# Optimization experiments

Measured on AMD Instinct MI355X. Metric: run time of the kernel, lower is better.

Reference implementation:

```python
import jax, jax.numpy as jnp
import numpy as np

N = 50000      # nodes
E = 800000     # edges (avg degree 16)
H = 4          # heads
C = 64         # per-head dim (= hidden_dim, TransformerConv out_channels)
D = H * C      # 256, concat output dim
VOCAB = 100


def setup_inputs() -> dict:
    key = jax.random.key(0)
    ks = jax.random.split(key, 16)
    f = lambda k, shape: (jax.random.normal(k, shape, jnp.float32) * 0.05)
    return {
        "x": jax.random.randint(ks[0], (N,), 0, VOCAB),
        "edge_index": jax.random.randint(ks[1], (2, E), 0, N),
        "embed": f(ks[2], (VOCAB, C)),        # node_embed table (hidden_dim=64)
        "Wq": f(ks[3], (C, D)), "bq": f(ks[4], (D,)),
        "Wk": f(ks[5], (C, D)), "bk": f(ks[6], (D,)),
        "Wv": f(ks[7], (C, D)), "bv": f(ks[8], (D,)),
        "Wskip": f(ks[9], (C, D)), "bskip": f(ks[10], (D,)),
        "Wbeta": f(ks[11], (3 * D, 1)),       # lin_beta has no bias in PyG
        "Wcoop": f(ks[12], (D, 1)), "bcoop": f(ks[13], (1,)),
        "Wanom": f(ks[14], (D, 1)), "banom": f(ks[15], (1,)),
    }


def _segment_softmax(logits, seg, num_segments):
    # logits: [E, H], seg: [E] destination-node ids
    m = jax.ops.segment_max(logits, seg, num_segments=num_segments)   # [N, H]
    ex = jnp.exp(logits - m[seg])
    s = jax.ops.segment_sum(ex, seg, num_segments=num_segments)       # [N, H]
    return ex / (s[seg] + 1e-16)


def _transformer_conv(h, src, dst, Wq, bq, Wk, bk, Wv, bv, Wskip, bskip, Wbeta):
    # h: [N, C] node features; src->dst edges; PyG TransformerConv(beta=True)
    q = (h @ Wq + bq).reshape(N, H, C)
    k = (h @ Wk + bk).reshape(N, H, C)
    v = (h @ Wv + bv).reshape(N, H, C)
    # per-edge attention logits: query of dst, key of src
    logits = (q[dst] * k[src]).sum(-1) / np.sqrt(C)    # [E, H]
    alpha = _segment_softmax(logits, dst, N)           # softmax over in-edges of dst
    msg = v[src] * alpha[..., None]                    # [E, H, C]
    out = jax.ops.segment_sum(msg, dst, num_segments=N).reshape(N, D)
    # beta-gated skip connection
    x_r = h @ Wskip + bskip                            # [N, D]
    beta = jax.nn.sigmoid(jnp.concatenate([out, x_r, out - x_r], axis=-1) @ Wbeta)
    return beta * x_r + (1.0 - beta) * out             # [N, D]


def reference(x, edge_index, embed, Wq, bq, Wk, bk, Wv, bv,
              Wskip, bskip, Wbeta, Wcoop, bcoop, Wanom, banom):
    h = embed[x]                                       # long input -> embedding
    src, dst = edge_index[0], edge_index[1]
    h = _transformer_conv(h, src, dst, Wq, bq, Wk, bk, Wv, bv, Wskip, bskip, Wbeta)
    h = jax.nn.relu(h)                                 # dropout is identity (eval)
    cooperation = jax.nn.sigmoid(h @ Wcoop + bcoop)    # [N, 1]
    anomaly = jax.nn.sigmoid(h @ Wanom + banom)        # [N, 1]
    return cooperation, anomaly, h
```

## Files before the change

### kernel.cpp

```cpp
#include <hip/hip_runtime.h>
#include <hip/hip_bf16.h>

typedef __hip_bfloat16 bf16;

#define NN 50000
#define EE 800000
#define VOCABSZ 100
#define DD 256
#define NW 25
#define MAXD 64
#define NBUCK 500
#define BNODES 100
#define AWG 512
#define PCAP 24

static __device__ __forceinline__ float b2f(bf16 v) { return __bfloat162float(v); }

static __device__ __forceinline__ float ldf(const void* p, int i, int isf32) {
  if (isf32) return ((const float*)p)[i];
  return b2f(((const bf16*)p)[i]);
}

static __device__ __forceinline__ int block_detect(const unsigned short* e16) {
  __shared__ int f;
  if (threadIdx.x == 0) f = 0;
  __syncthreads();
  unsigned int ex = (e16[threadIdx.x] >> 7) & 0xFF;
  unsigned long long any = __ballot(ex >= 128);
  if ((threadIdx.x & 63) == 0 && any) atomicOr(&f, 1);
  __syncthreads();
  return f;
}

__global__ void k_build_tables(const void* __restrict__ embed,
    const void* __restrict__ Wq, const void* __restrict__ bq,
    const void* __restrict__ Wk, const void* __restrict__ bk,
    const void* __restrict__ Wv, const void* __restrict__ bv,
    const void* __restrict__ Ws, const void* __restrict__ bs,
    const void* __restrict__ Wbeta,
    const void* __restrict__ Wcoop, const void* __restrict__ bcoop,
    const void* __restrict__ Wanom, const void* __restrict__ banom,
    float* __restrict__ Qt, float* __restrict__ Kt,
    bf16* __restrict__ VtH, bf16* __restrict__ StH,
    float* __restrict__ Wf, int* __restrict__ flag)
{
  __shared__ float e[64];
  int isf32 = block_detect((const unsigned short*)embed);
  int t = threadIdx.x;

  if (blockIdx.y == 4) {
    if (blockIdx.x != 0) return;
    Wf[t]       = ldf(Wbeta, t, isf32)       + ldf(Wbeta, 512 + t, isf32);
    Wf[256 + t] = ldf(Wbeta, 256 + t, isf32) - ldf(Wbeta, 512 + t, isf32);
    Wf[512 + t] = ldf(Wcoop, t, isf32);
    Wf[768 + t] = ldf(Wanom, t, isf32);
    if (t == 0) {
      Wf[1024] = ldf(bcoop, 0, isf32);
      Wf[1025] = ldf(banom, 0, isf32);
      flag[0] = isf32;
    }
    return;
  }

  int row = blockIdx.x;
  if (t < 64) e[t] = ldf(embed, row * 64 + t, isf32);
  __syncthreads();
  const void* W; const void* b;
  switch (blockIdx.y) {
    case 0:  W = Wq; b = bq; break;
    case 1:  W = Wk; b = bk; break;
    case 2:  W = Wv; b = bv; break;
    default: W = Ws; b = bs; break;
  }
  float acc;
  if (isf32) {
    const float* w32 = (const float*)W;
    acc = ((const float*)b)[t];
    #pragma unroll 8
    for (int c = 0; c < 64; ++c) acc = fmaf(e[c], w32[c * DD + t], acc);
  } else {
    const bf16* w16 = (const bf16*)W;
    acc = b2f(((const bf16*)b)[t]);
    #pragma unroll 8
    for (int c = 0; c < 64; ++c) acc = fmaf(e[c], b2f(w16[c * DD + t]), acc);
  }
  switch (blockIdx.y) {
    case 0:  Qt[row * DD + t] = acc; break;
    case 1:  Kt[row * DD + t] = acc; break;
    case 2:  VtH[row * DD + t] = __float2bfloat16(acc); break;
    default: StH[row * DD + t] = __float2bfloat16(acc); break;
  }
}

__global__ void k_build_logits(const float* __restrict__ Qt, const float* __restrict__ Kt,
                               float* __restrict__ Et)
{
  __shared__ float q[DD];
  int a = blockIdx.x;
  q[threadIdx.x] = Qt[a * DD + threadIdx.x];
  __syncthreads();
  for (int idx = threadIdx.x; idx < VOCABSZ * 4; idx += 256) {
    int b = idx >> 2, h = idx & 3;
    const float* kk = Kt + b * DD + h * 64;
    const float* qq = q + h * 64;
    float acc = 0.f;
    #pragma unroll 8
    for (int c = 0; c < 64; ++c) acc += qq[c] * kk[c];
    Et[(a * VOCABSZ + b) * 4 + h] = __expf(acc * 0.125f);
  }
}

__global__ __launch_bounds__(256) void k_scatter2(
    const int* __restrict__ src, const int* __restrict__ dst,
    const int* __restrict__ x,
    unsigned char* __restrict__ cnt, unsigned short* __restrict__ seg)
{
  __shared__ unsigned int cur[NBUCK];
  const int t = threadIdx.x;
  for (int i = t; i < NBUCK; i += 256) cur[i] = 0;
  __syncthreads();
  const int per = (EE + AWG - 1) / AWG;
  const int e0 = blockIdx.x * per;
  int e1 = e0 + per; if (e1 > EE) e1 = EE;
  const size_t wbase = (size_t)blockIdx.x * NBUCK;
  for (int i = e0 + t; i < e1; i += 256) {
    unsigned d = (unsigned)dst[i];
    unsigned b = d / (unsigned)BNODES;
    unsigned dl = d - b * BNODES;
    unsigned xv = (unsigned)x[src[i]];
    unsigned pos = atomicAdd(&cur[b], 1u);
    if (pos < PCAP)
      seg[(wbase + b) * PCAP + pos] = (unsigned short)(dl | (xv << 7));
  }
  __syncthreads();
  for (int i = t; i < NBUCK; i += 256) {
    unsigned c = cur[i]; if (c > PCAP) c = PCAP;
    cnt[wbase + i] = (unsigned char)c;
  }
}

__global__ __launch_bounds__(256) void k_lists(
    const unsigned char* __restrict__ cnt, const unsigned short* __restrict__ seg,
    int* __restrict__ deg, unsigned short* __restrict__ ell16)
{
  __shared__ unsigned int hist[BNODES * NW];
  const int b = blockIdx.x;
  const int t = threadIdx.x;
  for (int i = t; i < BNODES * NW; i += 256) hist[i] = 0;
  __syncthreads();
  for (int w = t; w < AWG; w += 256) {
    const size_t sbase = ((size_t)w * NBUCK + b);
    unsigned c = cnt[sbase];
    const unsigned short* sp = seg + sbase * PCAP;
    for (unsigned i = 0; i < c; ++i) {
      unsigned r = sp[i];
      unsigned dl = r & 127u, xv = r >> 7;
      atomicAdd(&hist[dl * NW + (xv >> 2)], 1u << ((xv & 3) * 8));
    }
  }
  __syncthreads();
  if (t < BNODES) {
    int n = b * BNODES + t;
    const unsigned int* cw = hist + t * NW;
    unsigned short* dp = ell16 + (size_t)n * MAXD;
    int k = 0;
    #pragma unroll
    for (int w = 0; w < NW; ++w) {
      unsigned word = cw[w];
      if (!word) continue;
      #pragma unroll
      for (int bb = 0; bb < 4; ++bb) {
        unsigned c = (word >> (8 * bb)) & 255u;
        if (c) { if (k < MAXD) dp[k] = (unsigned short)((unsigned)(w * 4 + bb) | (c << 8)); k++; }
      }
    }
    deg[n] = (k < MAXD) ? k : MAXD;
  }
}

__global__ __launch_bounds__(256) void k_node(
    const int* __restrict__ x, const int* __restrict__ deg,
    const unsigned short* __restrict__ ell16,
    const bf16* __restrict__ VtH, const bf16* __restrict__ StH,
    const float* __restrict__ Et, const float* __restrict__ Wf,
    void* __restrict__ out, const int* __restrict__ flag)
{
  const int t = threadIdx.x;
  const int lane = t & 63;
  const int wv = t >> 6;
  const int l31 = lane & 31;
  const int hbase = lane & 32;
  const int n = blockIdx.x * 8 + wv * 2 + (lane >> 5);
  const int cb = l31 << 3;
  const int head = l31 >> 3;

  const int xd = x[n];
  const int dgn = deg[n];
  const int dgA = __shfl(dgn, 0, 64);
  const int dgB = __shfl(dgn, 32, 64);
  const int dmax = max(dgA, dgB);

  unsigned int mye = (l31 < dgn) ? (unsigned int)ell16[(size_t)n * MAXD + l31] : 0u;

  union BF8U { uint4 u; bf16 h[8]; };
  BF8U xru; xru.u = *reinterpret_cast<const uint4*>(StH + xd * DD + cb);
  const float4 wo0 = *reinterpret_cast<const float4*>(Wf + cb);
  const float4 wo1 = *reinterpret_cast<const float4*>(Wf + cb + 4);
  const float4 wx0 = *reinterpret_cast<const float4*>(Wf + 256 + cb);
  const float4 wx1 = *reinterpret_cast<const float4*>(Wf + 256 + cb + 4);

  const float* __restrict__ Erow = Et + xd * (VOCABSZ * 4) + head;

  float s = 0.f;
  float o0 = 0.f, o1 = 0.f, o2 = 0.f, o3 = 0.f;
  float o4 = 0.f, o5 = 0.f, o6 = 0.f, o7 = 0.f;

  const int j1 = (dmax < 32) ? dmax : 32;
  #pragma unroll 4
  for (int j = 0; j < j1; ++j) {
    unsigned int en = (unsigned int)__shfl((int)mye, hbase + j, 64);
    int xs = (int)(en & 255u);
    float e = (float)(en >> 8) * Erow[xs << 2];
    s += e;
    BF8U vv; vv.u = *reinterpret_cast<const uint4*>(VtH + xs * DD + cb);
    o0 = fmaf(e, b2f(vv.h[0]), o0); o1 = fmaf(e, b2f(vv.h[1]), o1);
    o2 = fmaf(e, b2f(vv.h[2]), o2); o3 = fmaf(e, b2f(vv.h[3]), o3);
    o4 = fmaf(e, b2f(vv.h[4]), o4); o5 = fmaf(e, b2f(vv.h[5]), o5);
    o6 = fmaf(e, b2f(vv.h[6]), o6); o7 = fmaf(e, b2f(vv.h[7]), o7);
  }
  if (dmax > 32) {
    unsigned int mye2 = (l31 + 32 < dgn) ? (unsigned int)ell16[(size_t)n * MAXD + 32 + l31] : 0u;
    for (int j = 32; j < dmax; ++j) {
      unsigned int en = (unsigned int)__shfl((int)mye2, hbase + (j - 32), 64);
      int xs = (int)(en & 255u);
      float e = (float)(en >> 8) * Erow[xs << 2];
      s += e;
      BF8U vv; vv.u = *reinterpret_cast<const uint4*>(VtH + xs * DD + cb);
      o0 = fmaf(e, b2f(vv.h[0]), o0); o1 = fmaf(e, b2f(vv.h[1]), o1);
      o2 = fmaf(e, b2f(vv.h[2]), o2); o3 = fmaf(e, b2f(vv.h[3]), o3);
      o4 = fmaf(e, b2f(vv.h[4]), o4); o5 = fmaf(e, b2f(vv.h[5]), o5);
      o6 = fmaf(e, b2f(vv.h[6]), o6); o7 = fmaf(e, b2f(vv.h[7]), o7);
    }
  }

  const float inv = 1.f / (s + 1e-16f);
  float o[8] = { o0*inv, o1*inv, o2*inv, o3*inv, o4*inv, o5*inv, o6*inv, o7*inv };
  float xr[8];
  #pragma unroll
  for (int j = 0; j < 8; ++j) xr[j] = b2f(xru.h[j]);

  float bp = o[0]*wo0.x + o[1]*wo0.y + o[2]*wo0.z + o[3]*wo0.w
           + o[4]*wo1.x + o[5]*wo1.y + o[6]*wo1.z + o[7]*wo1.w
           + xr[0]*wx0.x + xr[1]*wx0.y + xr[2]*wx0.z + xr[3]*wx0.w
           + xr[4]*wx1.x + xr[5]*wx1.y + xr[6]*wx1.z + xr[7]*wx1.w;
  #pragma unroll
  for (int m = 16; m >= 1; m >>= 1) bp += __shfl_xor(bp, m, 64);
  const float beta = 1.f / (1.f + __expf(-bp));

  const float4 wc0 = *reinterpret_cast<const float4*>(Wf + 512 + cb);
  const float4 wc1 = *reinterpret_cast<const float4*>(Wf + 512 + cb + 4);
  const float4 wa0 = *reinterpret_cast<const float4*>(Wf + 768 + cb);
  const float4 wa1 = *reinterpret_cast<const float4*>(Wf + 768 + cb + 4);
  const float wcv[8] = { wc0.x, wc0.y, wc0.z, wc0.w, wc1.x, wc1.y, wc1.z, wc1.w };
  const float wav[8] = { wa0.x, wa0.y, wa0.z, wa0.w, wa1.x, wa1.y, wa1.z, wa1.w };

  float h[8];
  float pc = 0.f, pa = 0.f;
  #pragma unroll
  for (int j = 0; j < 8; ++j) {
    float hv = beta * xr[j] + (1.f - beta) * o[j];
    hv = fmaxf(hv, 0.f);
    h[j] = hv;
    pc = fmaf(hv, wcv[j], pc);
    pa = fmaf(hv, wav[j], pa);
  }
  #pragma unroll
  for (int m = 16; m >= 1; m >>= 1) {
    pc += __shfl_xor(pc, m, 64);
    pa += __shfl_xor(pa, m, 64);
  }
  const float coop = 1.f / (1.f + __expf(-(pc + Wf[1024])));
  const float anom = 1.f / (1.f + __expf(-(pa + Wf[1025])));

  if (flag[0]) {
    float* fo = (float*)out;
    if (l31 == 0) { fo[n] = coop; fo[NN + n] = anom; }
    float4* hp = reinterpret_cast<float4*>(fo + 2 * NN + (size_t)n * DD + cb);
    hp[0] = make_float4(h[0], h[1], h[2], h[3]);
    hp[1] = make_float4(h[4], h[5], h[6], h[7]);
  } else {
    bf16* bo = (bf16*)out;
    if (l31 == 0) { bo[n] = __float2bfloat16(coop); bo[NN + n] = __float2bfloat16(anom); }
    struct alignas(16) BF8S { bf16 v[8]; } hb;
    #pragma unroll
    for (int j = 0; j < 8; ++j) hb.v[j] = __float2bfloat16(h[j]);
    *reinterpret_cast<BF8S*>(bo + 2 * NN + (size_t)n * DD + cb) = hb;
  }
}

extern "C" void kernel_launch(void* const* d_in, const int* in_sizes, int n_in,
                              void* d_out, int out_size, void* d_ws, size_t ws_size,
                              hipStream_t stream) {
  (void)in_sizes; (void)n_in; (void)out_size; (void)ws_size;
  const int*  x     = (const int*)d_in[0];
  const int*  ei    = (const int*)d_in[1];
  const void* embed = d_in[2];
  const void* Wq = d_in[3];  const void* bq = d_in[4];
  const void* Wk = d_in[5];  const void* bk = d_in[6];
  const void* Wv = d_in[7];  const void* bv = d_in[8];
  const void* Ws = d_in[9];  const void* bs = d_in[10];
  const void* Wbeta = d_in[11];
  const void* Wcoop = d_in[12]; const void* bcoop = d_in[13];
  const void* Wanom = d_in[14]; const void* banom = d_in[15];
  const int* src = ei;
  const int* dst = ei + EE;

  char* base = (char*)d_ws;
  size_t pos = 0;
  auto take = [&](size_t bytes) -> char* {
    char* p = base + pos;
    pos = (pos + bytes + 255) & ~(size_t)255;
    return p;
  };
  float* Qt  = (float*)take(VOCABSZ * DD * sizeof(float));
  float* Kt  = (float*)take(VOCABSZ * DD * sizeof(float));
  bf16*  VtH = (bf16*)take(VOCABSZ * DD * sizeof(bf16));
  bf16*  StH = (bf16*)take(VOCABSZ * DD * sizeof(bf16));
  float* Et  = (float*)take(VOCABSZ * VOCABSZ * 4 * sizeof(float));
  float* Wf  = (float*)take(1026 * sizeof(float));
  int*   deg = (int*)take(NN * sizeof(int));
  int*   flag= (int*)take(256 * sizeof(int));
  unsigned char*  cnt   = (unsigned char*)take((size_t)AWG * NBUCK);
  unsigned short* seg   = (unsigned short*)take((size_t)AWG * NBUCK * PCAP * sizeof(unsigned short));
  unsigned short* ell16 = (unsigned short*)take((size_t)NN * MAXD * sizeof(unsigned short));

  k_build_tables<<<dim3(VOCABSZ, 5), 256, 0, stream>>>(
      embed, Wq, bq, Wk, bk, Wv, bv, Ws, bs,
      Wbeta, Wcoop, bcoop, Wanom, banom,
      Qt, Kt, VtH, StH, Wf, flag);
  k_build_logits<<<VOCABSZ, 256, 0, stream>>>(Qt, Kt, Et);

  k_scatter2<<<AWG, 256, 0, stream>>>(src, dst, x, cnt, seg);
  k_lists<<<NBUCK, 256, 0, stream>>>(cnt, seg, deg, ell16);

  k_node<<<NN / 8, 256, 0, stream>>>(x, deg, ell16, VtH, StH, Et, Wf, d_out, flag);
}
```

Measured before the change: 169.9 us.

## Vectorize edge loads in scatter and transpose bucket layout to bucket-major

The scatter kernel now reads src/dst as int4 so each thread handles four edges, with 500 workgroups of exactly 1600 edges each. The per-workgroup segment and count arrays are transposed to bucket-major order, so the list-building kernel reads contiguous memory for its bucket. This aims to cut load instruction count and improve coalescing in the consumer, at the cost of scattered writes in the producer. It assumes the edge count divides evenly and that src/dst are 16-byte aligned.

```diff
diff --git a/kernel.cpp b/kernel.cpp
--- a/kernel.cpp
+++ b/kernel.cpp
@@ -11,7 +11,8 @@
 #define MAXD 64
 #define NBUCK 500
 #define BNODES 100
-#define AWG 512
+#define AWG 500
+#define EPW 1600
 #define PCAP 24
 
 static __device__ __forceinline__ float b2f(bf16 v) { return __bfloat162float(v); }
@@ -111,31 +112,39 @@
 }
 
 __global__ __launch_bounds__(256) void k_scatter2(
-    const int* __restrict__ src, const int* __restrict__ dst,
+    const int4* __restrict__ src4, const int4* __restrict__ dst4,
     const int* __restrict__ x,
     unsigned char* __restrict__ cnt, unsigned short* __restrict__ seg)
 {
   __shared__ unsigned int cur[NBUCK];
   const int t = threadIdx.x;
+  const unsigned w = blockIdx.x;
   for (int i = t; i < NBUCK; i += 256) cur[i] = 0;
   __syncthreads();
-  const int per = (EE + AWG - 1) / AWG;
-  const int e0 = blockIdx.x * per;
-  int e1 = e0 + per; if (e1 > EE) e1 = EE;
-  const size_t wbase = (size_t)blockIdx.x * NBUCK;
-  for (int i = e0 + t; i < e1; i += 256) {
-    unsigned d = (unsigned)dst[i];
-    unsigned b = d / (unsigned)BNODES;
-    unsigned dl = d - b * BNODES;
-    unsigned xv = (unsigned)x[src[i]];
-    unsigned pos = atomicAdd(&cur[b], 1u);
-    if (pos < PCAP)
-      seg[(wbase + b) * PCAP + pos] = (unsigned short)(dl | (xv << 7));
+  const int g0 = blockIdx.x * (EPW / 4);
+  for (int g = t; g < EPW / 4; g += 256) {
+    int4 s = src4[g0 + g];
+    int4 d = dst4[g0 + g];
+    int xv0 = x[s.x], xv1 = x[s.y], xv2 = x[s.z], xv3 = x[s.w];
+    unsigned b0 = (unsigned)d.x / BNODES, b1 = (unsigned)d.y / BNODES;
+    unsigned b2 = (unsigned)d.z / BNODES, b3 = (unsigned)d.w / BNODES;
+    unsigned p0 = atomicAdd(&cur[b0], 1u);
+    unsigned p1 = atomicAdd(&cur[b1], 1u);
+    unsigned p2 = atomicAdd(&cur[b2], 1u);
+    unsigned p3 = atomicAdd(&cur[b3], 1u);
+    if (p0 < PCAP) seg[((size_t)b0 * AWG + w) * PCAP + p0] =
+        (unsigned short)(((unsigned)d.x - b0 * BNODES) | ((unsigned)xv0 << 7));
+    if (p1 < PCAP) seg[((size_t)b1 * AWG + w) * PCAP + p1] =
+        (unsigned short)(((unsigned)d.y - b1 * BNODES) | ((unsigned)xv1 << 7));
+    if (p2 < PCAP) seg[((size_t)b2 * AWG + w) * PCAP + p2] =
+        (unsigned short)(((unsigned)d.z - b2 * BNODES) | ((unsigned)xv2 << 7));
+    if (p3 < PCAP) seg[((size_t)b3 * AWG + w) * PCAP + p3] =
+        (unsigned short)(((unsigned)d.w - b3 * BNODES) | ((unsigned)xv3 << 7));
   }
   __syncthreads();
   for (int i = t; i < NBUCK; i += 256) {
     unsigned c = cur[i]; if (c > PCAP) c = PCAP;
-    cnt[wbase + i] = (unsigned char)c;
+    cnt[(size_t)i * AWG + w] = (unsigned char)c;
   }
 }
 
@@ -149,7 +158,7 @@
   for (int i = t; i < BNODES * NW; i += 256) hist[i] = 0;
   __syncthreads();
   for (int w = t; w < AWG; w += 256) {
-    const size_t sbase = ((size_t)w * NBUCK + b);
+    const size_t sbase = (size_t)b * AWG + w;
     unsigned c = cnt[sbase];
     const unsigned short* sp = seg + sbase * PCAP;
     for (unsigned i = 0; i < c; ++i) {
@@ -340,7 +349,7 @@
       Qt, Kt, VtH, StH, Wf, flag);
   k_build_logits<<<VOCABSZ, 256, 0, stream>>>(Qt, Kt, Et);
 
-  k_scatter2<<<AWG, 256, 0, stream>>>(src, dst, x, cnt, seg);
+  k_scatter2<<<AWG, 256, 0, stream>>>((const int4*)src, (const int4*)dst, x, cnt, seg);
   k_lists<<<NBUCK, 256, 0, stream>>>(cnt, seg, deg, ell16);
 
   k_node<<<NN / 8, 256, 0, stream>>>(x, deg, ell16, VtH, StH, Et, Wf, d_out, flag);
```

Measured after the change: 165.1 us. 2.8% less time.
